# Performance work log

Hardware: AMD Instinct MI355X
Metric: run time of the kernel (lower is better)

## Reference

```python
import jax, jax.numpy as jnp
import numpy as np

N = 100000  # nodes
E = 1600000  # edges
F = 128      # nfeat == nclass (source constructs every layer as nfeat->nclass)


def setup_inputs() -> dict:
    key = jax.random.key(0)
    ks = jax.random.split(key, 8)
    x = jax.random.normal(ks[0], (N, F), dtype=jnp.float32)
    row = jax.random.randint(ks[1], (E,), 0, N)
    col = jax.random.randint(ks[2], (E,), 0, N)
    s = (1.0 / np.sqrt(F)).astype(np.float32) if hasattr(1.0/np.sqrt(F), 'astype') else 1.0/np.sqrt(F)
    s = 1.0 / np.sqrt(F)
    W0 = jax.random.uniform(ks[3], (F, F), jnp.float32, -s, s)
    b0 = jax.random.uniform(ks[4], (F,), jnp.float32, -s, s)
    W1 = jax.random.uniform(ks[5], (F, F), jnp.float32, -s, s)
    b1 = jax.random.uniform(ks[6], (F,), jnp.float32, -s, s)
    return {"x": x, "W0": W0, "b0": b0, "W1": W1, "b1": b1, "row": row, "col": col}


def _gcn_layer(h_in, W, b, row, col, dinv):
    # h = Linear(feat)
    h = h_in @ W + b
    # (D^-1/2 (A+I) D^-1/2) @ h, A in COO (row=i, col=j), A[i,j]=1
    coef = dinv[row] * dinv[col]                      # [E]
    msg = h[col] * coef[:, None]                       # [E, F] gather
    agg = jax.ops.segment_sum(msg, row, num_segments=N)
    agg = agg + (dinv * dinv)[:, None] * h             # self loops (identity)
    return agg


def reference(x, W0, b0, W1, b1, row, col):
    # D_hat = diag((A + I).sum(0)) -> column sums + 1
    deg = jax.ops.segment_sum(jnp.ones((E,), jnp.float32), col, num_segments=N) + 1.0
    dinv = deg ** -0.5
    h = _gcn_layer(x, W0, b0, row, col, dinv)
    h = jax.nn.relu(h)            # with_relu=True; dropout off (eval mode)
    h = _gcn_layer(h, W1, b1, row, col, dinv)
    return jax.nn.log_softmax(h, axis=1)
```

## Files before the change

kernel.cpp:

```cpp
#include <hip/hip_runtime.h>
#include <math.h>

#define FDIM 128
#define RPB 128
#define BSTRIDE 32
#define NBLK 256
#define MAXB 1024
#define CAP 4096

typedef __attribute__((ext_vector_type(8))) short short8;
typedef __attribute__((ext_vector_type(4))) float floatx4;

static __device__ __forceinline__ unsigned short f2bf(float f) {
    unsigned int u = __float_as_uint(f);
    u = (u + 0x7fff + ((u >> 16) & 1)) >> 16;
    return (unsigned short)u;
}

static __device__ __forceinline__ unsigned int cvtpk(float a, float b) {
    unsigned int r;
    asm("v_cvt_pk_bf16_f32 %0, %1, %2" : "=v"(r) : "v"(a), "v"(b));
    return r;
}

static __device__ __forceinline__ void bf2f(unsigned int u, float& a, float& b) {
    a = __uint_as_float(u << 16);
    b = __uint_as_float(u & 0xffff0000u);
}


__global__ __launch_bounds__(256) void k_init(int* rbCnt, int nb, int* deg, int n, unsigned int* hsz,
                                              const float* __restrict__ W0, const float* __restrict__ W1,
                                              unsigned short* __restrict__ W0t, unsigned short* __restrict__ W1t) {
    const int b = blockIdx.x;
    const int tid = threadIdx.x;
    if (b == 0) {
        for (int i = tid; i < nb; i += 256) rbCnt[(size_t)i * BSTRIDE] = 0;
        if (tid < 64) hsz[tid] = 0u;
    } else if (b == 1 || b == 2) {
        const float* W = (b == 1) ? W0 : W1;
        unsigned short* Wt = (b == 1) ? W0t : W1t;
        for (int idx = tid; idx < FDIM * FDIM; idx += 256) {
            int k = idx >> 7, c = idx & 127;
            Wt[c * FDIM + k] = f2bf(W[idx]);
        }
    } else {
        int i = (b - 3) * 256 + tid;
        if (i < n) deg[i] = 0;
    }
}


__global__ __launch_bounds__(256) void k_scatter(const int* __restrict__ row, const int* __restrict__ col,
                                                 int* rbCnt, unsigned int* __restrict__ pairs,
                                                 int* deg, int nE, int nb) {
    __shared__ int rh[MAXB];
    __shared__ int rbase[MAXB];
    const int tid = threadIdx.x;
    const int cpb = (nE + NBLK - 1) / NBLK;
    const int e0 = blockIdx.x * cpb;
    int e1 = e0 + cpb; if (e1 > nE) e1 = nE;

    for (int i = tid; i < nb; i += 256) rh[i] = 0;
    __syncthreads();
    for (int e = e0 + tid; e < e1; e += 256)
        atomicAdd(&rh[row[e] >> 7], 1);
    __syncthreads();
    for (int i = tid; i < nb; i += 256) {
        rbase[i] = rh[i] ? (i * CAP + atomicAdd(&rbCnt[(size_t)i * BSTRIDE], rh[i])) : 0;
        rh[i] = 0;
    }
    __syncthreads();
    const int pmax = nb * CAP - 1;
    for (int e = e0 + tid; e < e1; e += 256) {
        int r = row[e];
        int c = col[e];
        int rb = r >> 7;
        int p = rbase[rb] + atomicAdd(&rh[rb], 1);
        if (p > pmax) p = pmax;
        pairs[p] = ((unsigned int)(r & (RPB - 1)) << 25) | (unsigned int)c;
        atomicAdd(&deg[c], 1);
    }
}


__global__ __launch_bounds__(256) void k_rowsort(const int* __restrict__ rbCnt,
                                                 const unsigned int* __restrict__ pairs,
                                                 const int* __restrict__ deg,
                                                 uint2* __restrict__ rse, float* __restrict__ dinv,
                                                 int* __restrict__ csr_col, int n, int nb) {
    __shared__ int hist[RPB];
    __shared__ int scan[RPB];
    __shared__ int lcur[RPB];
    const int b = blockIdx.x;
    const int tid = threadIdx.x;
    const int row0 = b * RPB;
    int cnt = rbCnt[(size_t)b * BSTRIDE]; if (cnt > CAP) cnt = CAP;
    const int start = b * CAP;
    const int endp = start + cnt;

    if (tid < RPB) hist[tid] = 0;
    __syncthreads();
    for (int i = start + tid; i < endp; i += 256)
        atomicAdd(&hist[pairs[i] >> 25], 1);
    __syncthreads();

    if (tid < RPB) scan[tid] = hist[tid];
    __syncthreads();
    for (int off = 1; off < RPB; off <<= 1) {
        int t = (tid < RPB && tid >= off) ? scan[tid - off] : 0;
        __syncthreads();
        if (tid < RPB) scan[tid] += t;
        __syncthreads();
    }
    if (tid < RPB) {
        int ex = start + scan[tid] - hist[tid];
        lcur[tid] = ex;
        int r = row0 + tid;
        if (r < n) {
            rse[r] = make_uint2((unsigned int)ex, (unsigned int)(ex + hist[tid]));
            dinv[r] = rsqrtf((float)deg[r] + 1.0f);
        }
    }
    __syncthreads();

    for (int i = start + tid; i < endp; i += 256) {
        unsigned int u = pairs[i];
        int pos = atomicAdd(&lcur[u >> 25], 1);
        csr_col[pos] = (int)(u & 0x1FFFFFFu);
    }
}


#define KH 64
#define LPAD 72

__global__ __launch_bounds__(256) void k_gemm_mfma(const void* __restrict__ Ain,
                                                   const unsigned short* __restrict__ Wt,
                                                   const float* __restrict__ bias,
                                                   const float* __restrict__ dinv,
                                                   unsigned int* __restrict__ outp, int n, int af32) {
    __shared__ unsigned short sA[128][LPAD];
    __shared__ unsigned short sW[128][LPAD];

    const unsigned short* A = (const unsigned short*)Ain;
    const float* Af = (const float*)Ain;

    const int tid = threadIdx.x;
    const int row0 = blockIdx.x * 128;
    const int wid = tid >> 6;
    const int lane = tid & 63;
    const int quad = lane >> 4;
    const int lq = lane & 15;
    const int wm = wid & 1;
    const int wn = wid >> 1;

    floatx4 acc[4][4];
#pragma unroll
    for (int i = 0; i < 4; i++)
#pragma unroll
        for (int j = 0; j < 4; j++) acc[i][j] = (floatx4){0.f, 0.f, 0.f, 0.f};

    for (int kh = 0; kh < 2; kh++) {
        if (kh) __syncthreads();
#pragma unroll
        for (int it = 0; it < 4; it++) {
            int f = tid + it * 256;
            int r = f >> 3;
            int c8 = (f & 7) * 8;
            int gr = row0 + r;
            if (af32) {
                float4 v0 = make_float4(0.f, 0.f, 0.f, 0.f);
                float4 v1 = make_float4(0.f, 0.f, 0.f, 0.f);
                if (gr < n) {
                    v0 = *(const float4*)&Af[(size_t)gr * FDIM + kh * KH + c8];
                    v1 = *(const float4*)&Af[(size_t)gr * FDIM + kh * KH + c8 + 4];
                }
                uint4 p;
                p.x = cvtpk(v0.x, v0.y);
                p.y = cvtpk(v0.z, v0.w);
                p.z = cvtpk(v1.x, v1.y);
                p.w = cvtpk(v1.z, v1.w);
                *(uint4*)&sA[r][c8] = p;
            } else {
                uint4 v = make_uint4(0u, 0u, 0u, 0u);
                if (gr < n) v = *(const uint4*)&A[(size_t)gr * FDIM + kh * KH + c8];
                *(uint4*)&sA[r][c8] = v;
            }
            uint4 wv = *(const uint4*)&Wt[(size_t)r * FDIM + kh * KH + c8];
            *(uint4*)&sW[r][c8] = wv;
        }
        __syncthreads();

#pragma unroll
        for (int kt = 0; kt < 2; kt++) {
            const int k0 = kt * 32 + quad * 8;
            short8 af[4], bf[4];
#pragma unroll
            for (int mt = 0; mt < 4; mt++)
                af[mt] = *(const short8*)&sA[wm * 64 + mt * 16 + lq][k0];
#pragma unroll
            for (int nt = 0; nt < 4; nt++)
                bf[nt] = *(const short8*)&sW[wn * 64 + nt * 16 + lq][k0];
#pragma unroll
            for (int mt = 0; mt < 4; mt++)
#pragma unroll
                for (int nt = 0; nt < 4; nt++)
                    acc[mt][nt] = __builtin_amdgcn_mfma_f32_16x16x32_bf16(af[mt], bf[nt], acc[mt][nt], 0, 0, 0);
        }
    }

    float bv[4];
#pragma unroll
    for (int nt = 0; nt < 4; nt++) bv[nt] = bias[wn * 64 + nt * 16 + lq];

#pragma unroll
    for (int mt = 0; mt < 4; mt++) {
#pragma unroll
        for (int r = 0; r < 4; r++) {
            int grow = row0 + wm * 64 + mt * 16 + quad * 4 + r;
            float di = (grow < n) ? dinv[grow] : 0.f;
#pragma unroll
            for (int nt = 0; nt < 4; nt++) {
                float v = (acc[mt][nt][r] + bv[nt]) * di;
                float pv = __shfl_xor(v, 1, 64);
                if (!(lq & 1) && grow < n) {
                    int col = wn * 64 + nt * 16 + lq;
                    outp[(size_t)grow * 64 + (col >> 1)] =
                        (unsigned int)f2bf(v) | ((unsigned int)f2bf(pv) << 16);
                }
            }
        }
    }
}


#define UACC(U) { float p_, q_; \
    bf2f(U.x, p_, q_); acc0 += p_; acc1 += q_; \
    bf2f(U.y, p_, q_); acc2 += p_; acc3 += q_; \
    bf2f(U.z, p_, q_); acc4 += p_; acc5 += q_; \
    bf2f(U.w, p_, q_); acc6 += p_; acc7 += q_; }

__global__ __launch_bounds__(256) void k_agg(const unsigned int* __restrict__ hs,
                                             const uint2* __restrict__ rse,
                                             const int* __restrict__ csr_col, const float* __restrict__ dinv,
                                             void* __restrict__ out, int n, int relu, int lsm, int obf) {
    int w = (blockIdx.x * 256 + threadIdx.x) >> 6;
    int lane = threadIdx.x & 63;
    if (w >= n) return;
    const int quad = lane >> 4;
    const int lq = lane & 15;

    const uint2 se = rse[w];
    int e = (int)se.x;
    const int end = (int)se.y;
    const float di = dinv[w];

    uint4 sv = make_uint4(0u, 0u, 0u, 0u);
    if (quad == 0) sv = *(const uint4*)&hs[(size_t)w * 64 + lq * 4];
    float acc0, acc1, acc2, acc3, acc4, acc5, acc6, acc7;
    bf2f(sv.x, acc0, acc1);
    bf2f(sv.y, acc2, acc3);
    bf2f(sv.z, acc4, acc5);
    bf2f(sv.w, acc6, acc7);

    const int zrow = n;

    while (e < end) {
        int cnt = end - e;
        if (cnt > 64) cnt = 64;
        int jv = (e + lane < end) ? csr_col[e + lane] : zrow;
        int nb8 = (cnt + 7) >> 3;
        for (int t = 0; t < nb8; t++) {
            int i0 = t * 8 + quad;
            int j0 = __shfl(jv, i0, 64);
            int j1 = __shfl(jv, i0 + 4, 64);
            uint4 u0 = *(const uint4*)&hs[(size_t)j0 * 64 + lq * 4];
            uint4 u1 = *(const uint4*)&hs[(size_t)j1 * 64 + lq * 4];
            UACC(u0)
            UACC(u1)
        }
        e += cnt;
    }

    acc0 += __shfl_xor(acc0, 16, 64); acc0 += __shfl_xor(acc0, 32, 64);
    acc1 += __shfl_xor(acc1, 16, 64); acc1 += __shfl_xor(acc1, 32, 64);
    acc2 += __shfl_xor(acc2, 16, 64); acc2 += __shfl_xor(acc2, 32, 64);
    acc3 += __shfl_xor(acc3, 16, 64); acc3 += __shfl_xor(acc3, 32, 64);
    acc4 += __shfl_xor(acc4, 16, 64); acc4 += __shfl_xor(acc4, 32, 64);
    acc5 += __shfl_xor(acc5, 16, 64); acc5 += __shfl_xor(acc5, 32, 64);
    acc6 += __shfl_xor(acc6, 16, 64); acc6 += __shfl_xor(acc6, 32, 64);
    acc7 += __shfl_xor(acc7, 16, 64); acc7 += __shfl_xor(acc7, 32, 64);

    acc0 *= di; acc1 *= di; acc2 *= di; acc3 *= di;
    acc4 *= di; acc5 *= di; acc6 *= di; acc7 *= di;
    if (relu) {
        acc0 = fmaxf(acc0, 0.f); acc1 = fmaxf(acc1, 0.f);
        acc2 = fmaxf(acc2, 0.f); acc3 = fmaxf(acc3, 0.f);
        acc4 = fmaxf(acc4, 0.f); acc5 = fmaxf(acc5, 0.f);
        acc6 = fmaxf(acc6, 0.f); acc7 = fmaxf(acc7, 0.f);
    }
    if (lsm) {
        float m = fmaxf(fmaxf(fmaxf(acc0, acc1), fmaxf(acc2, acc3)),
                        fmaxf(fmaxf(acc4, acc5), fmaxf(acc6, acc7)));
#pragma unroll
        for (int off = 1; off < 16; off <<= 1) m = fmaxf(m, __shfl_xor(m, off, 64));
        float s = ((expf(acc0 - m) + expf(acc1 - m)) + (expf(acc2 - m) + expf(acc3 - m))) +
                  ((expf(acc4 - m) + expf(acc5 - m)) + (expf(acc6 - m) + expf(acc7 - m)));
#pragma unroll
        for (int off = 1; off < 16; off <<= 1) s += __shfl_xor(s, off, 64);
        float lg = m + logf(s);
        acc0 -= lg; acc1 -= lg; acc2 -= lg; acc3 -= lg;
        acc4 -= lg; acc5 -= lg; acc6 -= lg; acc7 -= lg;
    }
    if (obf) {
        if (quad == 0) {
            uint4 o;
            o.x = (unsigned int)f2bf(acc0) | ((unsigned int)f2bf(acc1) << 16);
            o.y = (unsigned int)f2bf(acc2) | ((unsigned int)f2bf(acc3) << 16);
            o.z = (unsigned int)f2bf(acc4) | ((unsigned int)f2bf(acc5) << 16);
            o.w = (unsigned int)f2bf(acc6) | ((unsigned int)f2bf(acc7) << 16);
            *(uint4*)((unsigned int*)out + (size_t)w * 64 + lq * 4) = o;
        }
    } else {
        if (quad < 2) {
            float4 o = quad ? make_float4(acc4, acc5, acc6, acc7)
                            : make_float4(acc0, acc1, acc2, acc3);
            *(float4*)((float*)out + (size_t)w * 128 + lq * 8 + quad * 4) = o;
        }
    }
}


extern "C" void kernel_launch(void* const* d_in, const int* in_sizes, int n_in,
                              void* d_out, int out_size, void* d_ws, size_t ws_size,
                              hipStream_t stream) {
    const float* x  = (const float*)d_in[0];
    const float* W0 = (const float*)d_in[1];
    const float* b0 = (const float*)d_in[2];
    const float* W1 = (const float*)d_in[3];
    const float* b1 = (const float*)d_in[4];
    const int* row  = (const int*)d_in[5];
    const int* col  = (const int*)d_in[6];
    float* out = (float*)d_out;

    const int N = in_sizes[0] / FDIM;
    const int E = in_sizes[5];
    const int NB = (N + RPB - 1) / RPB;

    char* w = (char*)d_ws;
    size_t off = 0;
    auto alloc = [&](size_t bytes) {
        char* p = w + off;
        off += (bytes + 255) & ~(size_t)255;
        return p;
    };
    int* rbCnt   = (int*)alloc((size_t)NB * BSTRIDE * 4);
    float* dinv  = (float*)alloc((size_t)N * 4);
    int* deg     = (int*)alloc((size_t)N * 4);
    uint2* rse   = (uint2*)alloc((size_t)N * 8);
    int* csr_col = (int*)alloc((size_t)NB * CAP * 4);
    unsigned short* W0t = (unsigned short*)alloc((size_t)FDIM * FDIM * 2);
    unsigned short* W1t = (unsigned short*)alloc((size_t)FDIM * FDIM * 2);
    unsigned int* hs = (unsigned int*)alloc((size_t)(N + 1) * 64 * 4);
    size_t pairsSz = (size_t)NB * CAP * 4;
    size_t hbSz    = (size_t)N * 64 * 4;
    char* uni = (char*)alloc(pairsSz > hbSz ? pairsSz : hbSz);
    unsigned int* pairs = (unsigned int*)uni;
    unsigned int* hb = (unsigned int*)uni;

    const int gW = (N * 64 + 255) / 256;
    const int gG = (N + 127) / 128;
    const int gI = 3 + (N + 255) / 256;

    k_init<<<gI, 256, 0, stream>>>(rbCnt, NB, deg, N, hs + (size_t)N * 64, W0, W1, W0t, W1t);
    k_scatter<<<NBLK, 256, 0, stream>>>(row, col, rbCnt, pairs, deg, E, NB);
    k_rowsort<<<NB, 256, 0, stream>>>(rbCnt, pairs, deg, rse, dinv, csr_col, N, NB);

    k_gemm_mfma<<<gG, 256, 0, stream>>>((const void*)x, W0t, b0, dinv, hs, N, 1);
    k_agg<<<gW, 256, 0, stream>>>(hs, rse, csr_col, dinv, hb, N, 1, 0, 1);

    k_gemm_mfma<<<gG, 256, 0, stream>>>((const void*)hb, W1t, b1, dinv, hs, N, 0);
    k_agg<<<gW, 256, 0, stream>>>(hs, rse, csr_col, dinv, out, N, 0, 1, 0);
}
```

Baseline: 387.5 us.

## Compute degrees via column-bucketed local histograms instead of global atomics

Replaces the per-edge global atomicAdd on deg[col] with a second bucketing pass: each scatter block buckets edges by column block and writes a one-byte local column index, and the sort kernel builds per-block column histograms in shared memory to derive dinv. This removes 1.6M contended global atomics and the separate deg zeroing. The scatter grid also grows from 256 to 1024 blocks for more parallelism. The cost is extra shared-memory histograms, more global atomics on the bucket counters, and an extra byte array written and read.

```diff
diff --git a/kernel.cpp b/kernel.cpp
--- a/kernel.cpp
+++ b/kernel.cpp
@@ -4,7 +4,7 @@
 #define FDIM 128
 #define RPB 128
 #define BSTRIDE 32
-#define NBLK 256
+#define NBLK 1024
 #define MAXB 1024
 #define CAP 4096
 
@@ -29,80 +29,90 @@
 }
 
 
-__global__ __launch_bounds__(256) void k_init(int* rbCnt, int nb, int* deg, int n, unsigned int* hsz,
+__global__ __launch_bounds__(256) void k_init(int* rbCnt, int* cbCnt, int nb, unsigned int* hsz,
                                               const float* __restrict__ W0, const float* __restrict__ W1,
                                               unsigned short* __restrict__ W0t, unsigned short* __restrict__ W1t) {
     const int b = blockIdx.x;
     const int tid = threadIdx.x;
     if (b == 0) {
-        for (int i = tid; i < nb; i += 256) rbCnt[(size_t)i * BSTRIDE] = 0;
+        for (int i = tid; i < nb; i += 256) { rbCnt[(size_t)i * BSTRIDE] = 0; cbCnt[(size_t)i * BSTRIDE] = 0; }
         if (tid < 64) hsz[tid] = 0u;
-    } else if (b == 1 || b == 2) {
+    } else {
         const float* W = (b == 1) ? W0 : W1;
         unsigned short* Wt = (b == 1) ? W0t : W1t;
         for (int idx = tid; idx < FDIM * FDIM; idx += 256) {
             int k = idx >> 7, c = idx & 127;
             Wt[c * FDIM + k] = f2bf(W[idx]);
         }
-    } else {
-        int i = (b - 3) * 256 + tid;
-        if (i < n) deg[i] = 0;
     }
 }
 
 
 __global__ __launch_bounds__(256) void k_scatter(const int* __restrict__ row, const int* __restrict__ col,
-                                                 int* rbCnt, unsigned int* __restrict__ pairs,
-                                                 int* deg, int nE, int nb) {
+                                                 int* rbCnt, int* cbCnt,
+                                                 unsigned int* __restrict__ pairs,
+                                                 unsigned char* __restrict__ clocal, int nE, int nb) {
     __shared__ int rh[MAXB];
+    __shared__ int ch[MAXB];
     __shared__ int rbase[MAXB];
+    __shared__ int cbase[MAXB];
     const int tid = threadIdx.x;
     const int cpb = (nE + NBLK - 1) / NBLK;
     const int e0 = blockIdx.x * cpb;
     int e1 = e0 + cpb; if (e1 > nE) e1 = nE;
 
-    for (int i = tid; i < nb; i += 256) rh[i] = 0;
-    __syncthreads();
-    for (int e = e0 + tid; e < e1; e += 256)
+    for (int i = tid; i < nb; i += 256) { rh[i] = 0; ch[i] = 0; }
+    __syncthreads();
+    for (int e = e0 + tid; e < e1; e += 256) {
         atomicAdd(&rh[row[e] >> 7], 1);
+        atomicAdd(&ch[col[e] >> 7], 1);
+    }
     __syncthreads();
     for (int i = tid; i < nb; i += 256) {
         rbase[i] = rh[i] ? (i * CAP + atomicAdd(&rbCnt[(size_t)i * BSTRIDE], rh[i])) : 0;
+        cbase[i] = ch[i] ? (i * CAP + atomicAdd(&cbCnt[(size_t)i * BSTRIDE], ch[i])) : 0;
         rh[i] = 0;
+        ch[i] = 0;
     }
     __syncthreads();
     const int pmax = nb * CAP - 1;
     for (int e = e0 + tid; e < e1; e += 256) {
         int r = row[e];
         int c = col[e];
-        int rb = r >> 7;
+        int rb = r >> 7, cb = c >> 7;
         int p = rbase[rb] + atomicAdd(&rh[rb], 1);
         if (p > pmax) p = pmax;
         pairs[p] = ((unsigned int)(r & (RPB - 1)) << 25) | (unsigned int)c;
-        atomicAdd(&deg[c], 1);
-    }
-}
-
-
-__global__ __launch_bounds__(256) void k_rowsort(const int* __restrict__ rbCnt,
-                                                 const unsigned int* __restrict__ pairs,
-                                                 const int* __restrict__ deg,
-                                                 uint2* __restrict__ rse, float* __restrict__ dinv,
-                                                 int* __restrict__ csr_col, int n, int nb) {
+        int q = cbase[cb] + atomicAdd(&ch[cb], 1);
+        if (q > pmax) q = pmax;
+        clocal[q] = (unsigned char)(c & (RPB - 1));
+    }
+}
+
+
+__global__ __launch_bounds__(256) void k_sortdinv(const int* __restrict__ rbCnt, const int* __restrict__ cbCnt,
+                                                  const unsigned int* __restrict__ pairs,
+                                                  const unsigned char* __restrict__ clocal,
+                                                  uint2* __restrict__ rse, float* __restrict__ dinv,
+                                                  int* __restrict__ csr_col, int n, int nb) {
+    __shared__ int chist[RPB];
     __shared__ int hist[RPB];
     __shared__ int scan[RPB];
     __shared__ int lcur[RPB];
     const int b = blockIdx.x;
     const int tid = threadIdx.x;
     const int row0 = b * RPB;
-    int cnt = rbCnt[(size_t)b * BSTRIDE]; if (cnt > CAP) cnt = CAP;
+
+    int rcnt = rbCnt[(size_t)b * BSTRIDE]; if (rcnt > CAP) rcnt = CAP;
+    int ccnt = cbCnt[(size_t)b * BSTRIDE]; if (ccnt > CAP) ccnt = CAP;
     const int start = b * CAP;
-    const int endp = start + cnt;
-
-    if (tid < RPB) hist[tid] = 0;
-    __syncthreads();
-    for (int i = start + tid; i < endp; i += 256)
+
+    if (tid < RPB) { hist[tid] = 0; chist[tid] = 0; }
+    __syncthreads();
+    for (int i = start + tid; i < start + rcnt; i += 256)
         atomicAdd(&hist[pairs[i] >> 25], 1);
+    for (int i = start + tid; i < start + ccnt; i += 256)
+        atomicAdd(&chist[(int)clocal[i]], 1);
     __syncthreads();
 
     if (tid < RPB) scan[tid] = hist[tid];
@@ -119,12 +129,12 @@
         int r = row0 + tid;
         if (r < n) {
             rse[r] = make_uint2((unsigned int)ex, (unsigned int)(ex + hist[tid]));
-            dinv[r] = rsqrtf((float)deg[r] + 1.0f);
-        }
-    }
-    __syncthreads();
-
-    for (int i = start + tid; i < endp; i += 256) {
+            dinv[r] = rsqrtf((float)chist[tid] + 1.0f);
+        }
+    }
+    __syncthreads();
+
+    for (int i = start + tid; i < start + rcnt; i += 256) {
         unsigned int u = pairs[i];
         int pos = atomicAdd(&lcur[u >> 25], 1);
         csr_col[pos] = (int)(u & 0x1FFFFFFu);
@@ -356,26 +366,28 @@
         return p;
     };
     int* rbCnt   = (int*)alloc((size_t)NB * BSTRIDE * 4);
+    int* cbCnt   = (int*)alloc((size_t)NB * BSTRIDE * 4);
     float* dinv  = (float*)alloc((size_t)N * 4);
-    int* deg     = (int*)alloc((size_t)N * 4);
     uint2* rse   = (uint2*)alloc((size_t)N * 8);
     int* csr_col = (int*)alloc((size_t)NB * CAP * 4);
     unsigned short* W0t = (unsigned short*)alloc((size_t)FDIM * FDIM * 2);
     unsigned short* W1t = (unsigned short*)alloc((size_t)FDIM * FDIM * 2);
     unsigned int* hs = (unsigned int*)alloc((size_t)(N + 1) * 64 * 4);
     size_t pairsSz = (size_t)NB * CAP * 4;
+    size_t clocSz  = (size_t)NB * CAP;
+    size_t uniSz   = pairsSz + clocSz + 512;
     size_t hbSz    = (size_t)N * 64 * 4;
-    char* uni = (char*)alloc(pairsSz > hbSz ? pairsSz : hbSz);
+    char* uni = (char*)alloc(uniSz > hbSz ? uniSz : hbSz);
     unsigned int* pairs = (unsigned int*)uni;
+    unsigned char* clocal = (unsigned char*)(uni + pairsSz);
     unsigned int* hb = (unsigned int*)uni;
 
     const int gW = (N * 64 + 255) / 256;
     const int gG = (N + 127) / 128;
-    const int gI = 3 + (N + 255) / 256;
-
-    k_init<<<gI, 256, 0, stream>>>(rbCnt, NB, deg, N, hs + (size_t)N * 64, W0, W1, W0t, W1t);
-    k_scatter<<<NBLK, 256, 0, stream>>>(row, col, rbCnt, pairs, deg, E, NB);
-    k_rowsort<<<NB, 256, 0, stream>>>(rbCnt, pairs, deg, rse, dinv, csr_col, N, NB);
+
+    k_init<<<3, 256, 0, stream>>>(rbCnt, cbCnt, NB, hs + (size_t)N * 64, W0, W1, W0t, W1t);
+    k_scatter<<<NBLK, 256, 0, stream>>>(row, col, rbCnt, cbCnt, pairs, clocal, E, NB);
+    k_sortdinv<<<NB, 256, 0, stream>>>(rbCnt, cbCnt, pairs, clocal, rse, dinv, csr_col, N, NB);
 
     k_gemm_mfma<<<gG, 256, 0, stream>>>((const void*)x, W0t, b0, dinv, hs, N, 1);
     k_agg<<<gW, 256, 0, stream>>>(hs, rse, csr_col, dinv, hb, N, 1, 0, 1);
```

After: 412.9 us. 6.5% more time.
